# Kernel tuning notes

Hardware: AMD Instinct MI355X
Metric: run time of the kernel (lower is better)

## Reference

```python
import jax, jax.numpy as jnp
import numpy as np

D = 1024          # label_size / in_features
V = 100000        # vocab size
SHORTLIST = 10000 # cutoffs[0]
# tail clusters: (proj_dim, cluster_size) per div_value=2 schedule
TAILS = [(512, 10000), (256, 20000), (128, 40000), (64, 20000)]


def setup_inputs() -> dict:
    key = jax.random.key(0)
    ks = jax.random.split(key, 11)
    s = jnp.float32(0.02)
    inp = {
        "feature": jax.random.normal(ks[0], (D,), jnp.float32),
        "targets": jax.random.randint(ks[1], (4096,), 0, V),
        "head_w": jax.random.normal(ks[2], (SHORTLIST + len(TAILS), D), jnp.float32) * s,
    }
    for i, (h, c) in enumerate(TAILS):
        inp[f"t{i}p"] = jax.random.normal(ks[3 + 2 * i], (h, D), jnp.float32) * s
        inp[f"t{i}w"] = jax.random.normal(ks[4 + 2 * i], (c, h), jnp.float32) * s
    return inp


def reference(feature, targets, head_w, t0p, t0w, t1p, t1w, t2p, t2w, t3p, t3w):
    # head logits: [SHORTLIST + n_clusters]
    head_lp = jax.nn.log_softmax(head_w @ feature)
    parts = [head_lp[:SHORTLIST]]
    tails = [(t0p, t0w), (t1p, t1w), (t2p, t2w), (t3p, t3w)]
    for i, (p, w) in enumerate(tails):
        # two-stage low-rank projection: [h] then cluster logits [c]
        cl_lp = jax.nn.log_softmax(w @ (p @ feature)) + head_lp[SHORTLIST + i]
        parts.append(cl_lp)
    logprob = jnp.concatenate(parts)  # [V] full-vocab log-probabilities
    return -jnp.mean(logprob[targets])
```

## Files before the change

kernel.cpp:

```cpp
#include <hip/hip_runtime.h>
#include <math.h>

#define NHEAD     10004
#define OFF_HEAD  0
#define OFF_H0    10004
#define OFF_C0    10964
#define OFF_C1    20964
#define OFF_C2    40964
#define OFF_C3    80964
#define OFF_P     100964

#define P_C0   2501
#define P_C1   3751
#define P_C2   5001
#define P_C3   6251
#define NPAIR  6564
#define NBLK   1641

__device__ __forceinline__ float wave_sum(float v) {
  v += __shfl_xor(v, 32, 64);
  v += __shfl_xor(v, 16, 64);
  v += __shfl_xor(v, 8, 64);
  v += __shfl_xor(v, 4, 64);
  v += __shfl_xor(v, 2, 64);
  v += __shfl_xor(v, 1, 64);
  return v;
}

__device__ __forceinline__ float dot4(float4 a, float4 c) {
  return a.x * c.x + a.y * c.y + a.z * c.z + a.w * c.w;
}

__global__ __launch_bounds__(256) void proj_kernel(
    const float* __restrict__ feat,
    const float* __restrict__ p0, const float* __restrict__ p1,
    const float* __restrict__ p2, const float* __restrict__ p3,
    float* __restrict__ ws) {
  __shared__ __align__(16) float sf[1024];
  ((float4*)sf)[threadIdx.x] = ((const float4*)feat)[threadIdx.x];
  __syncthreads();
  const float4* sf4 = (const float4*)sf;
  const int lane = threadIdx.x & 63;
  const int pr = blockIdx.x * 4 + (threadIdx.x >> 6);
  const float* src;
  if (pr < 512)      src = p0 + (size_t)pr * 1024;
  else if (pr < 768) src = p1 + (size_t)(pr - 512) * 1024;
  else if (pr < 896) src = p2 + (size_t)(pr - 768) * 1024;
  else               src = p3 + (size_t)(pr - 896) * 1024;
  const float4* src4 = (const float4*)src;
  float4 ld[4];
#pragma unroll
  for (int j = 0; j < 4; ++j) ld[j] = src4[lane + j * 64];
  float acc = 0.f;
#pragma unroll
  for (int j = 0; j < 4; ++j) acc += dot4(ld[j], sf4[lane + j * 64]);
  acc = wave_sum(acc);
  if (lane == 0) ws[NHEAD + pr] = acc;
}

__global__ __launch_bounds__(256, 3) void main_kernel(
    const float* __restrict__ feat, const float* __restrict__ head_w,
    const float* __restrict__ w0, const float* __restrict__ w1,
    const float* __restrict__ w2, const float* __restrict__ w3,
    float* __restrict__ ws) {
  __shared__ __align__(16) float sh[1984];
  const int t = threadIdx.x;
  ((float4*)sh)[t] = ((const float4*)feat)[t];
  if (t < 240) ((float4*)(sh + 1024))[t] = ((const float4*)(ws + OFF_H0))[t];
  __syncthreads();
  const int lane = t & 63;
  const int w = blockIdx.x * 4 + (t >> 6);
  float esum = 0.f;

  if (w < P_C0) {
    const float4* sf4 = (const float4*)sh;
    const float4* base = (const float4*)head_w + (size_t)w * 1024;
    float4 ld[16];
#pragma unroll
    for (int j = 0; j < 16; ++j) ld[j] = base[j * 64 + lane];
    float a[4];
#pragma unroll
    for (int k = 0; k < 4; ++k) {
      float s = 0.f;
#pragma unroll
      for (int j = 0; j < 4; ++j) s += dot4(ld[4 * k + j], sf4[lane + j * 64]);
      a[k] = s;
    }
    const int r0 = w * 4;
#pragma unroll
    for (int k = 0; k < 4; ++k) {
      float s = wave_sum(a[k]);
      if (lane == 0) ws[OFF_HEAD + r0 + k] = s;
      esum += expf(s);
    }
  } else if (w < P_C1) {
    const float4* h4 = (const float4*)(sh + 1024);
    const float4 cv0 = h4[lane], cv1 = h4[lane + 64];
    const int v = w - P_C0, r0 = v * 8;
    const float4* base = (const float4*)w0 + (size_t)v * 1024;
    float4 ld[16];
#pragma unroll
    for (int j = 0; j < 16; ++j) ld[j] = base[j * 64 + lane];
#pragma unroll
    for (int k = 0; k < 8; ++k) {
      float a = dot4(ld[2 * k], cv0) + dot4(ld[2 * k + 1], cv1);
      a = wave_sum(a);
      if (lane == 0) ws[OFF_C0 + r0 + k] = a;
      esum += expf(a);
    }
  } else if (w < P_C2) {
    const float4 cv = ((const float4*)(sh + 1536))[lane];
    const int v = w - P_C1, r0 = v * 16;
    const float4* base = (const float4*)w1 + (size_t)v * 1024;
    float4 ld[16];
#pragma unroll
    for (int j = 0; j < 16; ++j) ld[j] = base[j * 64 + lane];
#pragma unroll
    for (int k = 0; k < 16; ++k) {
      float a = wave_sum(dot4(ld[k], cv));
      if (lane == 0) ws[OFF_C1 + r0 + k] = a;
      esum += expf(a);
    }
  } else if (w < P_C3) {
    const float4 cv = ((const float4*)(sh + 1792))[lane & 31];
    const int v = w - P_C2, r0 = v * 32;
    const float4* base = (const float4*)w2 + (size_t)v * 1024;
    float4 ld[16];
#pragma unroll
    for (int j = 0; j < 16; ++j) ld[j] = base[j * 64 + lane];
#pragma unroll
    for (int p = 0; p < 16; ++p) {
      float a = dot4(ld[p], cv);
      a += __shfl_xor(a, 1, 64);
      a += __shfl_xor(a, 2, 64);
      a += __shfl_xor(a, 4, 64);
      a += __shfl_xor(a, 8, 64);
      a += __shfl_xor(a, 16, 64);
      if ((lane & 31) == 0) ws[OFF_C2 + r0 + 2 * p + (lane >> 5)] = a;
      esum += expf(a);
    }
    esum += __shfl_xor(esum, 32, 64);
  } else {
    const float4 cv = ((const float4*)(sh + 1920))[lane & 15];
    const int v = w - P_C3, r0 = v * 64;
    const float4* base = (const float4*)w3 + (size_t)v * 1024;
    const bool full = (r0 + 64) <= 20000;
    const float4* base2 = full ? base + 512 : base;
    float4 ld[16];
#pragma unroll
    for (int j = 0; j < 8; ++j) ld[j] = base[j * 64 + lane];
#pragma unroll
    for (int j = 0; j < 8; ++j) ld[8 + j] = base2[j * 64 + lane];
#pragma unroll
    for (int p = 0; p < 8; ++p) {
      float a = dot4(ld[p], cv);
      a += __shfl_xor(a, 1, 64);
      a += __shfl_xor(a, 2, 64);
      a += __shfl_xor(a, 4, 64);
      a += __shfl_xor(a, 8, 64);
      if ((lane & 15) == 0) ws[OFF_C3 + r0 + 4 * p + (lane >> 4)] = a;
      esum += expf(a);
    }
    if (full) {
#pragma unroll
      for (int p = 0; p < 8; ++p) {
        float a = dot4(ld[8 + p], cv);
        a += __shfl_xor(a, 1, 64);
        a += __shfl_xor(a, 2, 64);
        a += __shfl_xor(a, 4, 64);
        a += __shfl_xor(a, 8, 64);
        if ((lane & 15) == 0) ws[OFF_C3 + r0 + 32 + 4 * p + (lane >> 4)] = a;
        esum += expf(a);
      }
    }
    esum += __shfl_xor(esum, 16, 64);
    esum += __shfl_xor(esum, 32, 64);
  }
  if (lane == 0) ws[OFF_P + w] = esum;
}

__global__ __launch_bounds__(1024) void finalize_kernel(
    const int* __restrict__ targets, float* __restrict__ ws,
    float* __restrict__ out) {
  const int tid = threadIdx.x;
  const int wv = tid >> 6, lane = tid & 63;
  float tv[4]; int sg[4];
#pragma unroll
  for (int it = 0; it < 4; ++it) {
    int tgt = targets[tid + it * 1024];
    int addr = tgt + ((tgt >= 10000) ? 964 : 0);
    tv[it] = ws[addr];
    sg[it] = (tgt >= 10000) + (tgt >= 20000) + (tgt >= 40000) + (tgt >= 80000);
  }
  float a0 = 0.f, a1 = 0.f, a2 = 0.f, a3 = 0.f, a4 = 0.f;
#pragma unroll
  for (int it = 0; it < 7; ++it) {
    int i = tid + it * 1024;
    if (i < NPAIR) {
      float v = ws[OFF_P + i];
      if (i < P_C0)      a0 += v;
      else if (i < P_C1) a1 += v;
      else if (i < P_C2) a2 += v;
      else if (i < P_C3) a3 += v;
      else               a4 += v;
    }
  }
  a0 = wave_sum(a0); a1 = wave_sum(a1); a2 = wave_sum(a2);
  a3 = wave_sum(a3); a4 = wave_sum(a4);
  __shared__ float r5[16][5];
  __shared__ float slse[5];
  if (lane == 0) { r5[wv][0] = a0; r5[wv][1] = a1; r5[wv][2] = a2; r5[wv][3] = a3; r5[wv][4] = a4; }
  __syncthreads();
  if (tid < 5) {
    float s = 0.f;
#pragma unroll
    for (int w = 0; w < 16; ++w) s += r5[w][tid];
    slse[tid] = logf(s);
  }
  __syncthreads();
  const float lse0 = slse[0], lse1 = slse[1], lse2 = slse[2], lse3 = slse[3], lse4 = slse[4];
  const float g0 = ws[10000] - lse0, g1 = ws[10001] - lse0;
  const float g2 = ws[10002] - lse0, g3 = ws[10003] - lse0;
  float s = 0.f;
#pragma unroll
  for (int it = 0; it < 4; ++it) {
    int e = sg[it];
    float lseS = (e == 0) ? lse0 : (e == 1) ? lse1 : (e == 2) ? lse2 : (e == 3) ? lse3 : lse4;
    float gS   = (e == 0) ? 0.f  : (e == 1) ? g0   : (e == 2) ? g1   : (e == 3) ? g2   : g3;
    s += tv[it] - lseS + gS;
  }
  s = wave_sum(s);
  if (lane == 0) r5[wv][0] = s;
  __syncthreads();
  if (tid == 0) {
    float tot = 0.f;
#pragma unroll
    for (int w = 0; w < 16; ++w) tot += r5[w][0];
    out[0] = -tot * (1.f / 4096.f);
  }
}

extern "C" void kernel_launch(void* const* d_in, const int* in_sizes, int n_in,
                              void* d_out, int out_size, void* d_ws, size_t ws_size,
                              hipStream_t stream) {
  const float* feat    = (const float*)d_in[0];
  const int*   targets = (const int*)d_in[1];
  const float* head_w  = (const float*)d_in[2];
  const float* t0p = (const float*)d_in[3];
  const float* t0w = (const float*)d_in[4];
  const float* t1p = (const float*)d_in[5];
  const float* t1w = (const float*)d_in[6];
  const float* t2p = (const float*)d_in[7];
  const float* t2w = (const float*)d_in[8];
  const float* t3p = (const float*)d_in[9];
  const float* t3w = (const float*)d_in[10];
  float* ws  = (float*)d_ws;
  float* out = (float*)d_out;

  proj_kernel<<<240, 256, 0, stream>>>(feat, t0p, t1p, t2p, t3p, ws);
  main_kernel<<<NBLK, 256, 0, stream>>>(feat, head_w, t0w, t1w, t2w, t3w, ws);
  finalize_kernel<<<1, 1024, 0, stream>>>(targets, ws, out);
}
```

Before: 160.6 us.

## Replace per-row wave reductions with butterfly transpose-reduce across lanes

Each wave used to reduce every output row separately with a full six-step shuffle reduction and one expf per row. Now a butterfly merge halves the number of partial sums at each shuffle stage, so one reduction pass leaves a different finished row in each lane. Results are stored by the lanes that own them, and expf runs once per lane in parallel. This cuts shuffle and transcendental work per wave, at the cost of more live registers and some lane-select logic. The partial last cluster-3 block is now handled by a validity mask instead of a branch.

```diff
diff --git a/kernel.cpp b/kernel.cpp
--- a/kernel.cpp
+++ b/kernel.cpp
@@ -29,6 +29,12 @@
 
 __device__ __forceinline__ float dot4(float4 a, float4 c) {
   return a.x * c.x + a.y * c.y + a.z * c.z + a.w * c.w;
+}
+
+__device__ __forceinline__ float mrg(float a, float b, int s, int lane) {
+  float as = __shfl_xor(a, s, 64);
+  float bs = __shfl_xor(b, s, 64);
+  return (lane & s) ? (b + bs) : (a + as);
 }
 
 __global__ __launch_bounds__(256) void proj_kernel(
@@ -70,7 +76,7 @@
   __syncthreads();
   const int lane = t & 63;
   const int w = blockIdx.x * 4 + (t >> 6);
-  float esum = 0.f;
+  float esum;
 
   if (w < P_C0) {
     const float4* sf4 = (const float4*)sh;
@@ -86,13 +92,17 @@
       for (int j = 0; j < 4; ++j) s += dot4(ld[4 * k + j], sf4[lane + j * 64]);
       a[k] = s;
     }
-    const int r0 = w * 4;
-#pragma unroll
-    for (int k = 0; k < 4; ++k) {
-      float s = wave_sum(a[k]);
-      if (lane == 0) ws[OFF_HEAD + r0 + k] = s;
-      esum += expf(s);
-    }
+    float u0 = mrg(a[0], a[1], 1, lane), u1 = mrg(a[2], a[3], 1, lane);
+    float y = mrg(u0, u1, 2, lane);
+    y += __shfl_xor(y, 4, 64);
+    y += __shfl_xor(y, 8, 64);
+    y += __shfl_xor(y, 16, 64);
+    y += __shfl_xor(y, 32, 64);
+    if (lane < 4) ws[OFF_HEAD + w * 4 + lane] = y;
+    float ev = expf(y);
+    ev += __shfl_xor(ev, 1, 64);
+    ev += __shfl_xor(ev, 2, 64);
+    esum = ev;
   } else if (w < P_C1) {
     const float4* h4 = (const float4*)(sh + 1024);
     const float4 cv0 = h4[lane], cv1 = h4[lane + 64];
@@ -101,13 +111,24 @@
     float4 ld[16];
 #pragma unroll
     for (int j = 0; j < 16; ++j) ld[j] = base[j * 64 + lane];
-#pragma unroll
-    for (int k = 0; k < 8; ++k) {
-      float a = dot4(ld[2 * k], cv0) + dot4(ld[2 * k + 1], cv1);
-      a = wave_sum(a);
-      if (lane == 0) ws[OFF_C0 + r0 + k] = a;
-      esum += expf(a);
-    }
+    float a[8];
+#pragma unroll
+    for (int k = 0; k < 8; ++k)
+      a[k] = dot4(ld[2 * k], cv0) + dot4(ld[2 * k + 1], cv1);
+    float u[4];
+#pragma unroll
+    for (int m = 0; m < 4; ++m) u[m] = mrg(a[2 * m], a[2 * m + 1], 1, lane);
+    float v0 = mrg(u[0], u[1], 2, lane), v1 = mrg(u[2], u[3], 2, lane);
+    float y = mrg(v0, v1, 4, lane);
+    y += __shfl_xor(y, 8, 64);
+    y += __shfl_xor(y, 16, 64);
+    y += __shfl_xor(y, 32, 64);
+    if (lane < 8) ws[OFF_C0 + r0 + lane] = y;
+    float ev = expf(y);
+    ev += __shfl_xor(ev, 1, 64);
+    ev += __shfl_xor(ev, 2, 64);
+    ev += __shfl_xor(ev, 4, 64);
+    esum = ev;
   } else if (w < P_C2) {
     const float4 cv = ((const float4*)(sh + 1536))[lane];
     const int v = w - P_C1, r0 = v * 16;
@@ -115,12 +136,28 @@
     float4 ld[16];
 #pragma unroll
     for (int j = 0; j < 16; ++j) ld[j] = base[j * 64 + lane];
-#pragma unroll
-    for (int k = 0; k < 16; ++k) {
-      float a = wave_sum(dot4(ld[k], cv));
-      if (lane == 0) ws[OFF_C1 + r0 + k] = a;
-      esum += expf(a);
-    }
+    float a[16];
+#pragma unroll
+    for (int k = 0; k < 16; ++k) a[k] = dot4(ld[k], cv);
+    float u[8];
+#pragma unroll
+    for (int m = 0; m < 8; ++m) u[m] = mrg(a[2 * m], a[2 * m + 1], 1, lane);
+    float v2[4];
+#pragma unroll
+    for (int m = 0; m < 4; ++m) v2[m] = mrg(u[2 * m], u[2 * m + 1], 2, lane);
+    float w2r[2];
+#pragma unroll
+    for (int m = 0; m < 2; ++m) w2r[m] = mrg(v2[2 * m], v2[2 * m + 1], 4, lane);
+    float y = mrg(w2r[0], w2r[1], 8, lane);
+    y += __shfl_xor(y, 16, 64);
+    y += __shfl_xor(y, 32, 64);
+    if (lane < 16) ws[OFF_C1 + r0 + lane] = y;
+    float ev = expf(y);
+    ev += __shfl_xor(ev, 1, 64);
+    ev += __shfl_xor(ev, 2, 64);
+    ev += __shfl_xor(ev, 4, 64);
+    ev += __shfl_xor(ev, 8, 64);
+    esum = ev;
   } else if (w < P_C3) {
     const float4 cv = ((const float4*)(sh + 1792))[lane & 31];
     const int v = w - P_C2, r0 = v * 32;
@@ -128,18 +165,29 @@
     float4 ld[16];
 #pragma unroll
     for (int j = 0; j < 16; ++j) ld[j] = base[j * 64 + lane];
-#pragma unroll
-    for (int p = 0; p < 16; ++p) {
-      float a = dot4(ld[p], cv);
-      a += __shfl_xor(a, 1, 64);
-      a += __shfl_xor(a, 2, 64);
-      a += __shfl_xor(a, 4, 64);
-      a += __shfl_xor(a, 8, 64);
-      a += __shfl_xor(a, 16, 64);
-      if ((lane & 31) == 0) ws[OFF_C2 + r0 + 2 * p + (lane >> 5)] = a;
-      esum += expf(a);
-    }
-    esum += __shfl_xor(esum, 32, 64);
+    float a[16];
+#pragma unroll
+    for (int p = 0; p < 16; ++p) a[p] = dot4(ld[p], cv);
+    float u[8];
+#pragma unroll
+    for (int m = 0; m < 8; ++m) u[m] = mrg(a[2 * m], a[2 * m + 1], 1, lane);
+    float v2[4];
+#pragma unroll
+    for (int m = 0; m < 4; ++m) v2[m] = mrg(u[2 * m], u[2 * m + 1], 2, lane);
+    float w2r[2];
+#pragma unroll
+    for (int m = 0; m < 2; ++m) w2r[m] = mrg(v2[2 * m], v2[2 * m + 1], 4, lane);
+    float y = mrg(w2r[0], w2r[1], 8, lane);
+    y += __shfl_xor(y, 16, 64);
+    int rr = 2 * (lane & 15) + (lane >> 5);
+    if (!(lane & 16)) ws[OFF_C2 + r0 + rr] = y;
+    float ev = expf(y);
+    ev += __shfl_xor(ev, 1, 64);
+    ev += __shfl_xor(ev, 2, 64);
+    ev += __shfl_xor(ev, 4, 64);
+    ev += __shfl_xor(ev, 8, 64);
+    ev += __shfl_xor(ev, 32, 64);
+    esum = ev;
   } else {
     const float4 cv = ((const float4*)(sh + 1920))[lane & 15];
     const int v = w - P_C3, r0 = v * 64;
@@ -151,30 +199,24 @@
     for (int j = 0; j < 8; ++j) ld[j] = base[j * 64 + lane];
 #pragma unroll
     for (int j = 0; j < 8; ++j) ld[8 + j] = base2[j * 64 + lane];
-#pragma unroll
-    for (int p = 0; p < 8; ++p) {
-      float a = dot4(ld[p], cv);
-      a += __shfl_xor(a, 1, 64);
-      a += __shfl_xor(a, 2, 64);
-      a += __shfl_xor(a, 4, 64);
-      a += __shfl_xor(a, 8, 64);
-      if ((lane & 15) == 0) ws[OFF_C3 + r0 + 4 * p + (lane >> 4)] = a;
-      esum += expf(a);
-    }
-    if (full) {
-#pragma unroll
-      for (int p = 0; p < 8; ++p) {
-        float a = dot4(ld[8 + p], cv);
-        a += __shfl_xor(a, 1, 64);
-        a += __shfl_xor(a, 2, 64);
-        a += __shfl_xor(a, 4, 64);
-        a += __shfl_xor(a, 8, 64);
-        if ((lane & 15) == 0) ws[OFF_C3 + r0 + 32 + 4 * p + (lane >> 4)] = a;
-        esum += expf(a);
-      }
-    }
-    esum += __shfl_xor(esum, 16, 64);
-    esum += __shfl_xor(esum, 32, 64);
+    float a[16];
+#pragma unroll
+    for (int p = 0; p < 16; ++p) a[p] = dot4(ld[p], cv);
+    float u[8];
+#pragma unroll
+    for (int m = 0; m < 8; ++m) u[m] = mrg(a[2 * m], a[2 * m + 1], 1, lane);
+    float v2[4];
+#pragma unroll
+    for (int m = 0; m < 4; ++m) v2[m] = mrg(u[2 * m], u[2 * m + 1], 2, lane);
+    float w2r[2];
+#pragma unroll
+    for (int m = 0; m < 2; ++m) w2r[m] = mrg(v2[2 * m], v2[2 * m + 1], 4, lane);
+    float y = mrg(w2r[0], w2r[1], 8, lane);
+    int rr = 4 * (lane & 15) + (lane >> 4);
+    bool valid = (r0 + rr) < 20000;
+    if (valid) ws[OFF_C3 + r0 + rr] = y;
+    float ev = valid ? expf(y) : 0.f;
+    esum = wave_sum(ev);
   }
   if (lane == 0) ws[OFF_P + w] = esum;
 }
```

Measured after the change: 157.8 us. Within noise of the previous version (-1.8%).

## Process two row-groups per wave and use transpose-style shuffle reductions

Applied to the files above, without the earlier changes.

Each wave now handles two 16 KB weight chunks, one from the first half and one from the second half of the pair index space, issuing 32 float4 loads before any compute to raise memory-level parallelism per wave. The grid is halved and occupancy hint reduced to 2 blocks per CU to fit the larger register footprint. Per-row wave_sum reductions are replaced by a butterfly merge (mrg) that reduces many rows at once, cutting shuffle count and letting expf run on several lanes in parallel. The cost is higher register pressure and fewer resident waves.

```diff
diff --git a/kernel.cpp b/kernel.cpp
--- a/kernel.cpp
+++ b/kernel.cpp
@@ -15,7 +15,8 @@
 #define P_C2   5001
 #define P_C3   6251
 #define NPAIR  6564
-#define NBLK   1641
+#define HALFW  3282
+#define NBLK   821
 
 __device__ __forceinline__ float wave_sum(float v) {
   v += __shfl_xor(v, 32, 64);
@@ -29,6 +30,12 @@
 
 __device__ __forceinline__ float dot4(float4 a, float4 c) {
   return a.x * c.x + a.y * c.y + a.z * c.z + a.w * c.w;
+}
+
+__device__ __forceinline__ float mrg(float a, float b, int s, int lane) {
+  float as = __shfl_xor(a, s, 64);
+  float bs = __shfl_xor(b, s, 64);
+  return (lane & s) ? (b + bs) : (a + as);
 }
 
 __global__ __launch_bounds__(256) void proj_kernel(
@@ -58,7 +65,162 @@
   if (lane == 0) ws[NHEAD + pr] = acc;
 }
 
-__global__ __launch_bounds__(256, 3) void main_kernel(
+__device__ __forceinline__ const float4* pair_base(
+    int w, const float* __restrict__ head_w, const float* __restrict__ w0,
+    const float* __restrict__ w1, const float* __restrict__ w2,
+    const float* __restrict__ w3) {
+  if (w < P_C0) return (const float4*)head_w + (size_t)w * 1024;
+  if (w < P_C1) return (const float4*)w0 + (size_t)(w - P_C0) * 1024;
+  if (w < P_C2) return (const float4*)w1 + (size_t)(w - P_C1) * 1024;
+  if (w < P_C3) return (const float4*)w2 + (size_t)(w - P_C2) * 1024;
+  return (const float4*)w3 + (size_t)(w - P_C3) * 1024;
+}
+
+#define COMPUTE_A(W, LD, ESUM) do {                                         \
+  if ((W) < P_C0) {                               \
+    const float4* sf4 = (const float4*)sh;                                  \
+    float a0 = 0.f, a1 = 0.f, a2 = 0.f, a3 = 0.f;                           \
+    _Pragma("unroll")                                                       \
+    for (int j = 0; j < 4; ++j) {                                           \
+      float4 f = sf4[lane + j * 64];                                        \
+      a0 += dot4(LD[j], f);  a1 += dot4(LD[4 + j], f);                      \
+      a2 += dot4(LD[8 + j], f); a3 += dot4(LD[12 + j], f);                  \
+    }                                                                       \
+    float u0 = mrg(a0, a1, 1, lane), u1 = mrg(a2, a3, 1, lane);             \
+    float y = mrg(u0, u1, 2, lane);                                         \
+    y += __shfl_xor(y, 4, 64);                                              \
+    y += __shfl_xor(y, 8, 64);                                              \
+    y += __shfl_xor(y, 16, 64);                                             \
+    y += __shfl_xor(y, 32, 64);                                             \
+    if (lane < 4) ws[OFF_HEAD + (W) * 4 + lane] = y;                        \
+    float ev = expf(y);                                                     \
+    ev += __shfl_xor(ev, 1, 64);                                            \
+    ev += __shfl_xor(ev, 2, 64);                                            \
+    ESUM = ev;                                                              \
+  } else {                                           \
+    const float4* h4 = (const float4*)(sh + 1024);                          \
+    const float4 cv0 = h4[lane], cv1 = h4[lane + 64];                       \
+    const int r0 = ((W) - P_C0) * 8;                                        \
+    float a[8];                                                             \
+    _Pragma("unroll")                                                       \
+    for (int k = 0; k < 8; ++k)                                             \
+      a[k] = dot4(LD[2 * k], cv0) + dot4(LD[2 * k + 1], cv1);               \
+    float u[4];                                                             \
+    _Pragma("unroll")                                                       \
+    for (int m = 0; m < 4; ++m) u[m] = mrg(a[2 * m], a[2 * m + 1], 1, lane);\
+    float v0 = mrg(u[0], u[1], 2, lane), v1 = mrg(u[2], u[3], 2, lane);     \
+    float y = mrg(v0, v1, 4, lane);                       \
+    y += __shfl_xor(y, 8, 64);                                              \
+    y += __shfl_xor(y, 16, 64);                                             \
+    y += __shfl_xor(y, 32, 64);                                             \
+    if (lane < 8) ws[OFF_C0 + r0 + lane] = y;                               \
+    float ev = expf(y);                                                     \
+    ev += __shfl_xor(ev, 1, 64);                                            \
+    ev += __shfl_xor(ev, 2, 64);                                            \
+    ev += __shfl_xor(ev, 4, 64);                                            \
+    ESUM = ev;                                                              \
+  }                                                                         \
+} while (0)
+
+#define COMPUTE_B(W, LD, ESUM) do {                                         \
+  if ((W) < P_C1) {                                  \
+    const float4* h4 = (const float4*)(sh + 1024);                          \
+    const float4 cv0 = h4[lane], cv1 = h4[lane + 64];                       \
+    const int r0 = ((W) - P_C0) * 8;                                        \
+    float a[8];                                                             \
+    _Pragma("unroll")                                                       \
+    for (int k = 0; k < 8; ++k)                                             \
+      a[k] = dot4(LD[2 * k], cv0) + dot4(LD[2 * k + 1], cv1);               \
+    float u[4];                                                             \
+    _Pragma("unroll")                                                       \
+    for (int m = 0; m < 4; ++m) u[m] = mrg(a[2 * m], a[2 * m + 1], 1, lane);\
+    float v0 = mrg(u[0], u[1], 2, lane), v1 = mrg(u[2], u[3], 2, lane);     \
+    float y = mrg(v0, v1, 4, lane);                                         \
+    y += __shfl_xor(y, 8, 64);                                              \
+    y += __shfl_xor(y, 16, 64);                                             \
+    y += __shfl_xor(y, 32, 64);                                             \
+    if (lane < 8) ws[OFF_C0 + r0 + lane] = y;                               \
+    float ev = expf(y);                                                     \
+    ev += __shfl_xor(ev, 1, 64);                                            \
+    ev += __shfl_xor(ev, 2, 64);                                            \
+    ev += __shfl_xor(ev, 4, 64);                                            \
+    ESUM = ev;                                                              \
+  } else if ((W) < P_C2) {                          \
+    const float4 cv = ((const float4*)(sh + 1536))[lane];                   \
+    const int r0 = ((W) - P_C1) * 16;                                       \
+    float a[16];                                                            \
+    _Pragma("unroll")                                                       \
+    for (int k = 0; k < 16; ++k) a[k] = dot4(LD[k], cv);                    \
+    float u[8];                                                             \
+    _Pragma("unroll")                                                       \
+    for (int m = 0; m < 8; ++m) u[m] = mrg(a[2 * m], a[2 * m + 1], 1, lane);\
+    float v2[4];                                                            \
+    _Pragma("unroll")                                                       \
+    for (int m = 0; m < 4; ++m) v2[m] = mrg(u[2 * m], u[2 * m + 1], 2, lane);\
+    float w2r[2];                                                           \
+    _Pragma("unroll")                                                       \
+    for (int m = 0; m < 2; ++m) w2r[m] = mrg(v2[2 * m], v2[2 * m + 1], 4, lane);\
+    float y = mrg(w2r[0], w2r[1], 8, lane);              \
+    y += __shfl_xor(y, 16, 64);                                             \
+    y += __shfl_xor(y, 32, 64);                                             \
+    if (lane < 16) ws[OFF_C1 + r0 + lane] = y;                              \
+    float ev = expf(y);                                                     \
+    ev += __shfl_xor(ev, 1, 64);                                            \
+    ev += __shfl_xor(ev, 2, 64);                                            \
+    ev += __shfl_xor(ev, 4, 64);                                            \
+    ev += __shfl_xor(ev, 8, 64);                                            \
+    ESUM = ev;                                                              \
+  } else if ((W) < P_C3) {                          \
+    const float4 cv = ((const float4*)(sh + 1792))[lane & 31];              \
+    const int r0 = ((W) - P_C2) * 32;                                       \
+    float a[16];                                                            \
+    _Pragma("unroll")                                                       \
+    for (int p = 0; p < 16; ++p) a[p] = dot4(LD[p], cv);                    \
+    float u[8];                                                             \
+    _Pragma("unroll")                                                       \
+    for (int m = 0; m < 8; ++m) u[m] = mrg(a[2 * m], a[2 * m + 1], 1, lane);\
+    float v2[4];                                                            \
+    _Pragma("unroll")                                                       \
+    for (int m = 0; m < 4; ++m) v2[m] = mrg(u[2 * m], u[2 * m + 1], 2, lane);\
+    float w2r[2];                                                           \
+    _Pragma("unroll")                                                       \
+    for (int m = 0; m < 2; ++m) w2r[m] = mrg(v2[2 * m], v2[2 * m + 1], 4, lane);\
+    float y = mrg(w2r[0], w2r[1], 8, lane);                \
+    y += __shfl_xor(y, 16, 64);             \
+    int rr = 2 * (lane & 15) + (lane >> 5);                                 \
+    if (!(lane & 16)) ws[OFF_C2 + r0 + rr] = y;                             \
+    float ev = expf(y);                                                     \
+    ev += __shfl_xor(ev, 1, 64);                                            \
+    ev += __shfl_xor(ev, 2, 64);                                            \
+    ev += __shfl_xor(ev, 4, 64);                                            \
+    ev += __shfl_xor(ev, 8, 64);                                            \
+    ev += __shfl_xor(ev, 32, 64);                                           \
+    ESUM = ev;                                                              \
+  } else {                                           \
+    const float4 cv = ((const float4*)(sh + 1920))[lane & 15];              \
+    const int r0 = ((W) - P_C3) * 64;                                       \
+    float a[16];                                                            \
+    _Pragma("unroll")                                                       \
+    for (int p = 0; p < 16; ++p) a[p] = dot4(LD[p], cv);                    \
+    float u[8];                                                             \
+    _Pragma("unroll")                                                       \
+    for (int m = 0; m < 8; ++m) u[m] = mrg(a[2 * m], a[2 * m + 1], 1, lane);\
+    float v2[4];                                                            \
+    _Pragma("unroll")                                                       \
+    for (int m = 0; m < 4; ++m) v2[m] = mrg(u[2 * m], u[2 * m + 1], 2, lane);\
+    float w2r[2];                                                           \
+    _Pragma("unroll")                                                       \
+    for (int m = 0; m < 2; ++m) w2r[m] = mrg(v2[2 * m], v2[2 * m + 1], 4, lane);\
+    float y = mrg(w2r[0], w2r[1], 8, lane);               \
+    int rr = 4 * (lane & 15) + (lane >> 4);      \
+    bool valid = (r0 + rr) < 20000;                                         \
+    if (valid) ws[OFF_C3 + r0 + rr] = y;                                    \
+    float ev = valid ? expf(y) : 0.f;                                       \
+    ESUM = wave_sum(ev);                                                    \
+  }                                                                         \
+} while (0)
+
+__global__ __launch_bounds__(256, 2) void main_kernel(
     const float* __restrict__ feat, const float* __restrict__ head_w,
     const float* __restrict__ w0, const float* __restrict__ w1,
     const float* __restrict__ w2, const float* __restrict__ w3,
@@ -69,114 +231,29 @@
   if (t < 240) ((float4*)(sh + 1024))[t] = ((const float4*)(ws + OFF_H0))[t];
   __syncthreads();
   const int lane = t & 63;
-  const int w = blockIdx.x * 4 + (t >> 6);
-  float esum = 0.f;
-
-  if (w < P_C0) {
-    const float4* sf4 = (const float4*)sh;
-    const float4* base = (const float4*)head_w + (size_t)w * 1024;
-    float4 ld[16];
-#pragma unroll
-    for (int j = 0; j < 16; ++j) ld[j] = base[j * 64 + lane];
-    float a[4];
-#pragma unroll
-    for (int k = 0; k < 4; ++k) {
-      float s = 0.f;
-#pragma unroll
-      for (int j = 0; j < 4; ++j) s += dot4(ld[4 * k + j], sf4[lane + j * 64]);
-      a[k] = s;
-    }
-    const int r0 = w * 4;
-#pragma unroll
-    for (int k = 0; k < 4; ++k) {
-      float s = wave_sum(a[k]);
-      if (lane == 0) ws[OFF_HEAD + r0 + k] = s;
-      esum += expf(s);
-    }
-  } else if (w < P_C1) {
-    const float4* h4 = (const float4*)(sh + 1024);
-    const float4 cv0 = h4[lane], cv1 = h4[lane + 64];
-    const int v = w - P_C0, r0 = v * 8;
-    const float4* base = (const float4*)w0 + (size_t)v * 1024;
-    float4 ld[16];
-#pragma unroll
-    for (int j = 0; j < 16; ++j) ld[j] = base[j * 64 + lane];
-#pragma unroll
-    for (int k = 0; k < 8; ++k) {
-      float a = dot4(ld[2 * k], cv0) + dot4(ld[2 * k + 1], cv1);
-      a = wave_sum(a);
-      if (lane == 0) ws[OFF_C0 + r0 + k] = a;
-      esum += expf(a);
-    }
-  } else if (w < P_C2) {
-    const float4 cv = ((const float4*)(sh + 1536))[lane];
-    const int v = w - P_C1, r0 = v * 16;
-    const float4* base = (const float4*)w1 + (size_t)v * 1024;
-    float4 ld[16];
-#pragma unroll
-    for (int j = 0; j < 16; ++j) ld[j] = base[j * 64 + lane];
-#pragma unroll
-    for (int k = 0; k < 16; ++k) {
-      float a = wave_sum(dot4(ld[k], cv));
-      if (lane == 0) ws[OFF_C1 + r0 + k] = a;
-      esum += expf(a);
-    }
-  } else if (w < P_C3) {
-    const float4 cv = ((const float4*)(sh + 1792))[lane & 31];
-    const int v = w - P_C2, r0 = v * 32;
-    const float4* base = (const float4*)w2 + (size_t)v * 1024;
-    float4 ld[16];
-#pragma unroll
-    for (int j = 0; j < 16; ++j) ld[j] = base[j * 64 + lane];
-#pragma unroll
-    for (int p = 0; p < 16; ++p) {
-      float a = dot4(ld[p], cv);
-      a += __shfl_xor(a, 1, 64);
-      a += __shfl_xor(a, 2, 64);
-      a += __shfl_xor(a, 4, 64);
-      a += __shfl_xor(a, 8, 64);
-      a += __shfl_xor(a, 16, 64);
-      if ((lane & 31) == 0) ws[OFF_C2 + r0 + 2 * p + (lane >> 5)] = a;
-      esum += expf(a);
-    }
-    esum += __shfl_xor(esum, 32, 64);
-  } else {
-    const float4 cv = ((const float4*)(sh + 1920))[lane & 15];
-    const int v = w - P_C3, r0 = v * 64;
-    const float4* base = (const float4*)w3 + (size_t)v * 1024;
-    const bool full = (r0 + 64) <= 20000;
-    const float4* base2 = full ? base + 512 : base;
-    float4 ld[16];
-#pragma unroll
-    for (int j = 0; j < 8; ++j) ld[j] = base[j * 64 + lane];
-#pragma unroll
-    for (int j = 0; j < 8; ++j) ld[8 + j] = base2[j * 64 + lane];
-#pragma unroll
-    for (int p = 0; p < 8; ++p) {
-      float a = dot4(ld[p], cv);
-      a += __shfl_xor(a, 1, 64);
-      a += __shfl_xor(a, 2, 64);
-      a += __shfl_xor(a, 4, 64);
-      a += __shfl_xor(a, 8, 64);
-      if ((lane & 15) == 0) ws[OFF_C3 + r0 + 4 * p + (lane >> 4)] = a;
-      esum += expf(a);
-    }
-    if (full) {
-#pragma unroll
-      for (int p = 0; p < 8; ++p) {
-        float a = dot4(ld[8 + p], cv);
-        a += __shfl_xor(a, 1, 64);
-        a += __shfl_xor(a, 2, 64);
-        a += __shfl_xor(a, 4, 64);
-        a += __shfl_xor(a, 8, 64);
-        if ((lane & 15) == 0) ws[OFF_C3 + r0 + 32 + 4 * p + (lane >> 4)] = a;
-        esum += expf(a);
-      }
-    }
-    esum += __shfl_xor(esum, 16, 64);
-    esum += __shfl_xor(esum, 32, 64);
-  }
-  if (lane == 0) ws[OFF_P + w] = esum;
+  const int wid = blockIdx.x * 4 + (t >> 6);
+  if (wid >= HALFW) return;
+
+  const int wA = wid, wB = wid + HALFW;
+  const float4* bA = pair_base(wA, head_w, w0, w1, w2, w3);
+  const float4* bB = pair_base(wB, head_w, w0, w1, w2, w3);
+  const float4* bB2 = bB + ((wB == NPAIR - 1) ? 0 : 512);
+
+  float4 ldA[16], ldB[16];
+#pragma unroll
+  for (int j = 0; j < 8; ++j) ldA[j] = bA[j * 64 + lane];
+#pragma unroll
+  for (int j = 0; j < 8; ++j) ldA[8 + j] = bA[512 + j * 64 + lane];
+#pragma unroll
+  for (int j = 0; j < 8; ++j) ldB[j] = bB[j * 64 + lane];
+#pragma unroll
+  for (int j = 0; j < 8; ++j) ldB[8 + j] = bB2[j * 64 + lane];
+  __builtin_amdgcn_sched_barrier(0);
+
+  float esA, esB;
+  COMPUTE_A(wA, ldA, esA);
+  COMPUTE_B(wB, ldB, esB);
+  if (lane == 0) { ws[OFF_P + wA] = esA; ws[OFF_P + wB] = esB; }
 }
 
 __global__ __launch_bounds__(1024) void finalize_kernel(
```

Measured after the change: 157.2 us. 2.2% less time.
